# Optimization experiments

Hardware: AMD Instinct MI355X
Metric: run time of the kernel (lower is better)

Reference implementation:

```python
import jax, jax.numpy as jnp
import numpy as np

N = 100000      # nodes
F_IN = 256      # num_node_features
E = 1600000     # edges (before self-loops)
DIMS = [F_IN, 128, 100, 32, 2]  # GCNConv layer widths


def _glorot(key, fan_in, fan_out):
    s = jnp.sqrt(6.0 / (fan_in + fan_out))
    return jax.random.uniform(key, (fan_in, fan_out), jnp.float32, -s, s)


def setup_inputs() -> dict:
    key = jax.random.key(0)
    ks = jax.random.split(key, 10)
    x = jax.random.normal(ks[0], (N, F_IN), jnp.float32)
    edge_index = jax.random.randint(ks[1], (2, E), 0, N, jnp.int32)
    inp = {"x": x, "edge_index": edge_index}
    for i in range(4):
        inp[f"W{i+1}"] = _glorot(ks[2 + 2 * i], DIMS[i], DIMS[i + 1])
        inp[f"b{i+1}"] = jnp.zeros((DIMS[i + 1],), jnp.float32)
    return inp


def reference(x, edge_index, W1, b1, W2, b2, W3, b3, W4, b4):
    n = x.shape[0]
    loops = jnp.arange(n, dtype=edge_index.dtype)
    src = jnp.concatenate([edge_index[0], loops])  # [E+N]
    dst = jnp.concatenate([edge_index[1], loops])
    # symmetric normalization: deg^-1/2[src] * deg^-1/2[dst] (self-loops included)
    deg = jax.ops.segment_sum(jnp.ones_like(src, x.dtype), dst, num_segments=n)
    dis = jax.lax.rsqrt(jnp.maximum(deg, 1.0))
    norm = (dis[src] * dis[dst])[:, None]  # [E+N, 1]

    def conv(h, W, b):
        h = h @ W                                      # [N, out]
        msg = h[src] * norm                            # gather + scale [E+N, out]
        return jax.ops.segment_sum(msg, dst, num_segments=n) + b

    h = jax.nn.leaky_relu(conv(x, W1, b1), negative_slope=0.1)
    h = jax.nn.leaky_relu(conv(h, W2, b2), negative_slope=0.1)
    h = jax.nn.leaky_relu(conv(h, W3, b3), negative_slope=0.1)
    h = conv(h, W4, b4)
    return jax.nn.softmax(h, axis=-1)
```

## Files before the change

### kernel.cpp

```cpp
#include <hip/hip_runtime.h>
#include <math.h>


typedef unsigned short ushort_t;
typedef unsigned int   uint_t;
typedef short  bf16x8 __attribute__((ext_vector_type(8)));
typedef float  f32x4  __attribute__((ext_vector_type(4)));

#define BKT_SHIFT 8
#define BKT_CAP   5120
#define BIN_CHUNK 4096

__device__ __forceinline__ ushort_t f2bf(float f) {
    union { float f; uint_t u; } v; v.f = f;
    uint_t u = v.u;
    u += 0x7fffu + ((u >> 16) & 1u);
    return (ushort_t)(u >> 16);
}
__device__ __forceinline__ float bflo(uint_t u) {
    union { uint_t q; float f; } v; v.q = u << 16; return v.f;
}
__device__ __forceinline__ float bfhi(uint_t u) {
    union { uint_t q; float f; } v; v.q = u & 0xffff0000u; return v.f;
}


__global__ __launch_bounds__(256) void bin_kernel(const int* __restrict__ srcArr,
                                                  const int* __restrict__ dstArr,
                                                  int* __restrict__ bkt_cursor,
                                                  uint2* __restrict__ staging,
                                                  int E, int nb) {
    __shared__ int hist[512];
    __shared__ int base[512];
    for (int b = threadIdx.x; b < 512; b += 256) hist[b] = 0;
    __syncthreads();
    const int e0 = blockIdx.x * BIN_CHUNK;
    #pragma unroll 4
    for (int k = 0; k < BIN_CHUNK / 256; ++k) {
        int e = e0 + k * 256 + threadIdx.x;
        if (e < E) atomicAdd(&hist[dstArr[e] >> BKT_SHIFT], 1);
    }
    __syncthreads();
    for (int b = threadIdx.x; b < nb; b += 256) {
        int h = hist[b];
        base[b] = h ? atomicAdd(&bkt_cursor[b], h) : 0;
    }
    __syncthreads();
    for (int b = threadIdx.x; b < 512; b += 256) hist[b] = 0;
    __syncthreads();
    #pragma unroll 4
    for (int k = 0; k < BIN_CHUNK / 256; ++k) {
        int e = e0 + k * 256 + threadIdx.x;
        if (e < E) {
            int s = srcArr[e], d = dstArr[e];
            int b = d >> BKT_SHIFT;
            int p = atomicAdd(&hist[b], 1);
            int idx = base[b] + p;
            if (idx < BKT_CAP)
                staging[(size_t)b * BKT_CAP + idx] = make_uint2((uint_t)s, (uint_t)d);
        }
    }
}

__global__ __launch_bounds__(512) void bucket_scan_kernel(const int* __restrict__ bkt_cursor,
                                                          int* __restrict__ bkt_base,
                                                          int* __restrict__ row_start,
                                                          int nbkt, int n) {
    __shared__ int buf[512];
    int v = ((int)threadIdx.x < nbkt) ? min(bkt_cursor[threadIdx.x], BKT_CAP) : 0;
    buf[threadIdx.x] = v;
    __syncthreads();
    for (int off = 1; off < 512; off <<= 1) {
        int t = (threadIdx.x >= (unsigned)off) ? buf[threadIdx.x - off] : 0;
        __syncthreads();
        buf[threadIdx.x] += t;
        __syncthreads();
    }
    if ((int)threadIdx.x < nbkt) bkt_base[threadIdx.x] = buf[threadIdx.x] - v;
    if ((int)threadIdx.x == nbkt - 1) row_start[n] = buf[threadIdx.x];
}

__global__ __launch_bounds__(256) void csr_build2_kernel(const uint2* __restrict__ staging,
                                                         const int* __restrict__ bkt_cursor,
                                                         const int* __restrict__ bkt_base,
                                                         int* __restrict__ row_start,
                                                         float* __restrict__ dis,
                                                         int* __restrict__ csr_src, int n) {
    __shared__ int cnt[256];
    __shared__ int buf[256];
    __shared__ int rsS[256];
    __shared__ int seg[BKT_CAP];
    const int t  = threadIdx.x;
    const int b  = blockIdx.x;
    const int lo = b << BKT_SHIFT;
    const int nl = min(256, n - lo);
    cnt[t] = 0;
    __syncthreads();
    const int cntE = min(bkt_cursor[b], BKT_CAP);
    for (int e = t; e < cntE; e += 256) {
        uint2 p = staging[(size_t)b * BKT_CAP + e];
        atomicAdd(&cnt[(int)p.y - lo], 1);
    }
    __syncthreads();
    const int v = cnt[t];
    buf[t] = v;
    __syncthreads();
    for (int off = 1; off < 256; off <<= 1) {
        int tt = (t >= off) ? buf[t - off] : 0;
        __syncthreads();
        buf[t] += tt;
        __syncthreads();
    }
    rsS[t] = buf[t] - v;
    const int sbase = bkt_base[b];
    if (t < nl) {
        row_start[lo + t] = sbase + (buf[t] - v);
        dis[lo + t] = rsqrtf((float)(v + 1));
    }
    cnt[t] = 0;
    __syncthreads();
    for (int e = t; e < cntE; e += 256) {
        uint2 p = staging[(size_t)b * BKT_CAP + e];
        int ln = (int)p.y - lo;
        int q  = atomicAdd(&cnt[ln], 1);
        seg[rsS[ln] + q] = (int)p.x;
    }
    __syncthreads();
    for (int i = t; i < cntE; i += 256) csr_src[sbase + i] = seg[i];
}


__global__ void cast_bf16_kernel(const float* __restrict__ in, ushort_t* __restrict__ out, int n8) {
    int i = blockIdx.x * blockDim.x + threadIdx.x;
    if (i >= n8) return;
    const float4 f0 = ((const float4*)in)[2 * i];
    const float4 f1 = ((const float4*)in)[2 * i + 1];
    uint4 o;
    o.x = (uint_t)f2bf(f0.x) | ((uint_t)f2bf(f0.y) << 16);
    o.y = (uint_t)f2bf(f0.z) | ((uint_t)f2bf(f0.w) << 16);
    o.z = (uint_t)f2bf(f1.x) | ((uint_t)f2bf(f1.y) << 16);
    o.w = (uint_t)f2bf(f1.z) | ((uint_t)f2bf(f1.w) << 16);
    ((uint4*)out)[i] = o;
}

__global__ void wt_all_kernel(const float* __restrict__ W1, const float* __restrict__ W2,
                              const float* __restrict__ W3,
                              ushort_t* __restrict__ Wt1, ushort_t* __restrict__ Wt2,
                              ushort_t* __restrict__ Wt3) {
    int idx = blockIdx.x * blockDim.x + threadIdx.x;
    if (idx < 32768) {
        int nn = idx >> 8, k = idx & 255;
        Wt1[idx] = f2bf(W1[(size_t)k * 128 + nn]);
    } else if (idx < 49152) {
        int j = idx - 32768;
        int nn = j >> 7, k = j & 127;
        float v = (nn < 100) ? W2[(size_t)k * 100 + nn] : 0.f;
        Wt2[j] = f2bf(v);
    } else if (idx < 57344) {
        int j = idx - 49152;
        int nn = j >> 7, k = j & 127;
        float v = (k < 100 && nn < 32) ? W3[(size_t)k * 32 + nn] : 0.f;
        Wt3[j] = f2bf(v);
    }
}

template <int NFR>
__global__ __launch_bounds__(256) void gemm_tile(const ushort_t* __restrict__ A,
                                                 const ushort_t* __restrict__ Bt,
                                                 ushort_t* __restrict__ C,
                                                 const float* __restrict__ dis,
                                                 int M, int K, int lda, int ldb, int ldc) {
    constexpr int BN = NFR * 32;
    __shared__ __attribute__((aligned(16))) ushort_t As[64][72];
    __shared__ __attribute__((aligned(16))) ushort_t Bs[BN][72];

    const int t    = threadIdx.x;
    const int lane = t & 63;
    const int w    = t >> 6;
    const int wm   = w >> 1, wn = w & 1;
    const int m0   = blockIdx.x * 64;
    const int rsel = lane & 15;
    const int q    = lane >> 4;

    f32x4 acc[2][NFR];
    #pragma unroll
    for (int mi = 0; mi < 2; ++mi)
        #pragma unroll
        for (int ni = 0; ni < NFR; ++ni) acc[mi][ni] = (f32x4){0.f, 0.f, 0.f, 0.f};

    const int srow = t >> 3;
    const int scol = (t & 7) * 8;

    for (int k0 = 0; k0 < K; k0 += 64) {
        #pragma unroll
        for (int it = 0; it < 2; ++it) {
            int r = srow + it * 32;
            int gm = m0 + r;
            bf16x8 v = {0, 0, 0, 0, 0, 0, 0, 0};
            if (gm < M) v = *(const bf16x8*)(A + (size_t)gm * lda + k0 + scol);
            *(bf16x8*)&As[r][scol] = v;
        }
        #pragma unroll
        for (int it = 0; it < BN / 32; ++it) {
            int r = srow + it * 32;
            bf16x8 v = *(const bf16x8*)(Bt + (size_t)r * ldb + k0 + scol);
            *(bf16x8*)&Bs[r][scol] = v;
        }
        __syncthreads();
        #pragma unroll
        for (int ks = 0; ks < 2; ++ks) {
            const int kc = ks * 32 + q * 8;
            bf16x8 af[2], bfr[NFR];
            #pragma unroll
            for (int mi = 0; mi < 2; ++mi)
                af[mi] = *(const bf16x8*)&As[wm * 32 + mi * 16 + rsel][kc];
            #pragma unroll
            for (int ni = 0; ni < NFR; ++ni)
                bfr[ni] = *(const bf16x8*)&Bs[wn * (BN / 2) + ni * 16 + rsel][kc];
            #pragma unroll
            for (int mi = 0; mi < 2; ++mi)
                #pragma unroll
                for (int ni = 0; ni < NFR; ++ni)
                    acc[mi][ni] = __builtin_amdgcn_mfma_f32_16x16x32_bf16(
                        bfr[ni], af[mi], acc[mi][ni], 0, 0, 0);
        }
        __syncthreads();
    }

    #pragma unroll
    for (int mi = 0; mi < 2; ++mi) {
        const int gm = m0 + wm * 32 + mi * 16 + rsel;
        if (gm >= M) continue;
        const float d = dis[gm];
        #pragma unroll
        for (int ni = 0; ni < NFR; ++ni) {
            uint2 o;
            o.x = (uint_t)f2bf(acc[mi][ni][0] * d) | ((uint_t)f2bf(acc[mi][ni][1] * d) << 16);
            o.y = (uint_t)f2bf(acc[mi][ni][2] * d) | ((uint_t)f2bf(acc[mi][ni][3] * d) << 16);
            *(uint2*)(C + (size_t)gm * ldc + wn * (BN / 2) + ni * 16 + q * 4) = o;
        }
    }
}

template <int F>
__global__ void aggregate128_kernel(const ushort_t* __restrict__ h, const int* __restrict__ row_start,
                                    const int* __restrict__ csr_src,
                                    const float* __restrict__ dis, const float* __restrict__ bias,
                                    ushort_t* __restrict__ out, int n) {
    const int lane = threadIdx.x & 63;
    const int grp  = lane >> 4;
    const int node = blockIdx.x * 16 + (int)(threadIdx.x >> 6) * 4 + grp;
    if (node >= n) return;
    const uint_t fbb = (uint_t)(lane & 15) << 4;
    const char* hb = (const char*)h;
    float a[8];
    #pragma unroll
    for (int j = 0; j < 8; ++j) a[j] = 0.f;

    int i = row_start[node];
    const int end = row_start[node + 1];

#define LOADR(S) (*(const uint4*)(hb + (((uint_t)(S) << 8) + fbb)))
#define ACC8(U)                                                     \
    do {                                                            \
        a[0] += bflo((U).x); a[1] += bfhi((U).x);                   \
        a[2] += bflo((U).y); a[3] += bfhi((U).y);                   \
        a[4] += bflo((U).z); a[5] += bfhi((U).z);                   \
        a[6] += bflo((U).w); a[7] += bfhi((U).w);                   \
    } while (0)

    for (; i + 4 <= end; i += 4) {
        int s0 = csr_src[i];
        int s1 = csr_src[i + 1];
        int s2 = csr_src[i + 2];
        int s3 = csr_src[i + 3];
        uint4 u0 = LOADR(s0);
        uint4 u1 = LOADR(s1);
        uint4 u2 = LOADR(s2);
        uint4 u3 = LOADR(s3);
        ACC8(u0); ACC8(u1); ACC8(u2); ACC8(u3);
    }
    for (; i < end; ++i) {
        uint4 u = LOADR(csr_src[i]);
        ACC8(u);
    }
    {
        uint4 su = LOADR(node);
        ACC8(su);
    }
    float dn = dis[node];
    const int fb = (lane & 15) * 8;
    #pragma unroll
    for (int j = 0; j < 8; ++j) {
        float b = (fb + j < F) ? bias[fb + j] : 0.f;
        float v = a[j] * dn + b;
        v = (v > 0.f) ? v : 0.1f * v;
        if (fb + j >= F) v = 0.f;
        a[j] = v;
    }
    uint4 o;
    o.x = (uint_t)f2bf(a[0]) | ((uint_t)f2bf(a[1]) << 16);
    o.y = (uint_t)f2bf(a[2]) | ((uint_t)f2bf(a[3]) << 16);
    o.z = (uint_t)f2bf(a[4]) | ((uint_t)f2bf(a[5]) << 16);
    o.w = (uint_t)f2bf(a[6]) | ((uint_t)f2bf(a[7]) << 16);
    *(uint4*)((char*)out + (((uint_t)node << 8) + fbb)) = o;
#undef ACC8
#undef LOADR
}

__global__ void aggregate32_kernel(const ushort_t* __restrict__ h, const int* __restrict__ row_start,
                                   const int* __restrict__ csr_src,
                                   const float* __restrict__ dis, const float* __restrict__ bias,
                                   ushort_t* __restrict__ out, int n) {
    int lane16 = threadIdx.x & 15;
    int node = blockIdx.x * (blockDim.x >> 4) + (threadIdx.x >> 4);
    if (node >= n) return;
    const uint_t fbb = (uint_t)lane16 << 2;
    const char* hb = (const char*)h;
#define LOADR32(S) (*(const uint_t*)(hb + (((uint_t)(S) << 6) + fbb)))
    uint_t v = LOADR32(node);
    float acc0 = bflo(v);
    float acc1 = bfhi(v);
    int i = row_start[node], end = row_start[node + 1];
    for (; i + 4 <= end; i += 4) {
        uint_t u0 = LOADR32(csr_src[i]);
        uint_t u1 = LOADR32(csr_src[i + 1]);
        uint_t u2 = LOADR32(csr_src[i + 2]);
        uint_t u3 = LOADR32(csr_src[i + 3]);
        acc0 += bflo(u0) + bflo(u1) + bflo(u2) + bflo(u3);
        acc1 += bfhi(u0) + bfhi(u1) + bfhi(u2) + bfhi(u3);
    }
    for (; i < end; ++i) {
        uint_t u = LOADR32(csr_src[i]);
        acc0 += bflo(u); acc1 += bfhi(u);
    }
#undef LOADR32
    float dn = dis[node];
    const int f0 = 2 * lane16;
    acc0 = acc0 * dn + bias[f0];
    acc1 = acc1 * dn + bias[f0 + 1];
    acc0 = (acc0 > 0.f) ? acc0 : 0.1f * acc0;
    acc1 = (acc1 > 0.f) ? acc1 : 0.1f * acc1;
    uint_t o = (uint_t)f2bf(acc0) | ((uint_t)f2bf(acc1) << 16);
    *(uint_t*)((char*)out + (((uint_t)node << 6) + fbb)) = o;
}

__global__ void gemm32x2_kernel(const ushort_t* __restrict__ H, const float* __restrict__ W4,
                                const float* __restrict__ dis, float* __restrict__ C, int n) {
    int node = blockIdx.x * blockDim.x + threadIdx.x;
    if (node >= n) return;
    const uint_t* row = (const uint_t*)(H + (size_t)node * 32);
    float a0 = 0.f, a1 = 0.f;
    #pragma unroll
    for (int k2 = 0; k2 < 16; ++k2) {
        uint_t u = row[k2];
        float x0 = bflo(u), x1 = bfhi(u);
        int k = 2 * k2;
        a0 += x0 * W4[k * 2]     + x1 * W4[(k + 1) * 2];
        a1 += x0 * W4[k * 2 + 1] + x1 * W4[(k + 1) * 2 + 1];
    }
    float d = dis[node];
    C[2 * (size_t)node]     = a0 * d;
    C[2 * (size_t)node + 1] = a1 * d;
}

__global__ void aggregate2_softmax_kernel(const float* __restrict__ h, const int* __restrict__ row_start,
                                          const int* __restrict__ csr_src,
                                          const float* __restrict__ dis, const float* __restrict__ bias,
                                          float* __restrict__ out, int n) {
    int node = blockIdx.x * blockDim.x + threadIdx.x;
    if (node >= n) return;
    const char* hb = (const char*)h;
    float a0 = h[2 * (size_t)node];
    float a1 = h[2 * (size_t)node + 1];
    int beg = row_start[node], end = row_start[node + 1];
    for (int i = beg; i < end; ++i) {
        uint_t off = (uint_t)csr_src[i] << 3;
        float2 u = *(const float2*)(hb + off);
        a0 += u.x;
        a1 += u.y;
    }
    float dn = dis[node];
    a0 = a0 * dn + bias[0];
    a1 = a1 * dn + bias[1];
    float m  = fmaxf(a0, a1);
    float e0 = expf(a0 - m), e1 = expf(a1 - m);
    float inv = 1.f / (e0 + e1);
    out[2 * (size_t)node]     = e0 * inv;
    out[2 * (size_t)node + 1] = e1 * inv;
}


extern "C" void kernel_launch(void* const* d_in, const int* in_sizes, int n_in,
                              void* d_out, int out_size, void* d_ws, size_t ws_size,
                              hipStream_t stream) {
    const float* x  = (const float*)d_in[0];
    const int*   ei = (const int*)d_in[1];
    const float* W1 = (const float*)d_in[2];
    const float* b1 = (const float*)d_in[3];
    const float* W2 = (const float*)d_in[4];
    const float* b2 = (const float*)d_in[5];
    const float* W3 = (const float*)d_in[6];
    const float* b3 = (const float*)d_in[7];
    const float* W4 = (const float*)d_in[8];
    const float* b4 = (const float*)d_in[9];

    const int N = in_sizes[0] / 256;
    const int E = in_sizes[1] / 2;
    const int* srcA = ei;
    const int* dstA = ei + E;
    const int nbkt = (N + 255) >> BKT_SHIFT;

    char* ws = (char*)d_ws;
    size_t off = 0;
    auto alloc = [&](size_t bytes) {
        void* p = ws + off;
        off = (off + bytes + 255) & ~(size_t)255;
        return p;
    };
    float*    dis        = (float*)alloc((size_t)N * 4);
    int*      row_start  = (int*)alloc((size_t)(N + 1) * 4);
    int*      bkt_cursor = (int*)alloc(512 * 4);
    int*      bkt_base   = (int*)alloc(512 * 4);
    int*      csr_src    = (int*)alloc((size_t)E * 4);
    uint2*    staging    = (uint2*)alloc((size_t)nbkt * BKT_CAP * 8);
    ushort_t* xb         = (ushort_t*)alloc((size_t)N * 256 * 2);
    ushort_t* bufA       = (ushort_t*)alloc((size_t)N * 128 * 2);
    ushort_t* bufB       = (ushort_t*)alloc((size_t)N * 128 * 2);
    float*    C4         = (float*)alloc((size_t)N * 2 * 4);
    ushort_t* Wt1        = (ushort_t*)alloc((size_t)128 * 256 * 2);
    ushort_t* Wt2        = (ushort_t*)alloc((size_t)128 * 128 * 2);
    ushort_t* Wt3        = (ushort_t*)alloc((size_t)64 * 128 * 2);
    (void)ws_size;

    hipMemsetAsync(bkt_cursor, 0, 512 * 4, stream);

    bin_kernel<<<(E + BIN_CHUNK - 1) / BIN_CHUNK, 256, 0, stream>>>(
        srcA, dstA, bkt_cursor, staging, E, nbkt);
    bucket_scan_kernel<<<1, 512, 0, stream>>>(bkt_cursor, bkt_base, row_start, nbkt, N);
    csr_build2_kernel<<<nbkt, 256, 0, stream>>>(staging, bkt_cursor, bkt_base,
                                                row_start, dis, csr_src, N);

    wt_all_kernel<<<(57344 + 255) / 256, 256, 0, stream>>>(W1, W2, W3, Wt1, Wt2, Wt3);
    const int n8 = N * 32;
    cast_bf16_kernel<<<(n8 + 255) / 256, 256, 0, stream>>>(x, xb, n8);

    const int gx = (N + 63) / 64;
    const int aggBlocks128 = (N + 15) / 16;
    const int aggBlocks32  = (N + 15) / 16;

    gemm_tile<4><<<gx, 256, 0, stream>>>(xb, Wt1, bufA, dis, N, 256, 256, 256, 128);
    aggregate128_kernel<128><<<aggBlocks128, 256, 0, stream>>>(
        bufA, row_start, csr_src, dis, b1, bufB, N);
    gemm_tile<4><<<gx, 256, 0, stream>>>(bufB, Wt2, bufA, dis, N, 128, 128, 128, 128);
    aggregate128_kernel<100><<<aggBlocks128, 256, 0, stream>>>(
        bufA, row_start, csr_src, dis, b2, bufB, N);
    gemm_tile<1><<<gx, 256, 0, stream>>>(bufB, Wt3, bufA, dis, N, 128, 128, 128, 32);
    aggregate32_kernel<<<aggBlocks32, 256, 0, stream>>>(
        bufA, row_start, csr_src, dis, b3, bufB, N);
    gemm32x2_kernel<<<(N + 255) / 256, 256, 0, stream>>>(bufB, W4, dis, C4, N);
    aggregate2_softmax_kernel<<<(N + 255) / 256, 256, 0, stream>>>(
        C4, row_start, csr_src, dis, b4, (float*)d_out, N);
}
```

Baseline: 299.3 us.

## Fuse fp32-to-bf16 cast into first GEMM, pack staging edges, unroll gathers

```diff
diff --git a/kernel.cpp b/kernel.cpp
--- a/kernel.cpp
+++ b/kernel.cpp
@@ -28,17 +28,24 @@
 __global__ __launch_bounds__(256) void bin_kernel(const int* __restrict__ srcArr,
                                                   const int* __restrict__ dstArr,
                                                   int* __restrict__ bkt_cursor,
-                                                  uint2* __restrict__ staging,
+                                                  uint_t* __restrict__ staging,
                                                   int E, int nb) {
     __shared__ int hist[512];
     __shared__ int base[512];
     for (int b = threadIdx.x; b < 512; b += 256) hist[b] = 0;
     __syncthreads();
     const int e0 = blockIdx.x * BIN_CHUNK;
-    #pragma unroll 4
-    for (int k = 0; k < BIN_CHUNK / 256; ++k) {
+    int sv[16], dv[16];
+    #pragma unroll
+    for (int k = 0; k < 16; ++k) {
         int e = e0 + k * 256 + threadIdx.x;
-        if (e < E) atomicAdd(&hist[dstArr[e] >> BKT_SHIFT], 1);
+        if (e < E) {
+            sv[k] = srcArr[e];
+            dv[k] = dstArr[e];
+            atomicAdd(&hist[dv[k] >> BKT_SHIFT], 1);
+        } else {
+            sv[k] = 0; dv[k] = -1;
+        }
     }
     __syncthreads();
     for (int b = threadIdx.x; b < nb; b += 256) {
@@ -48,16 +55,15 @@
     __syncthreads();
     for (int b = threadIdx.x; b < 512; b += 256) hist[b] = 0;
     __syncthreads();
-    #pragma unroll 4
-    for (int k = 0; k < BIN_CHUNK / 256; ++k) {
-        int e = e0 + k * 256 + threadIdx.x;
-        if (e < E) {
-            int s = srcArr[e], d = dstArr[e];
-            int b = d >> BKT_SHIFT;
+    #pragma unroll
+    for (int k = 0; k < 16; ++k) {
+        if (dv[k] >= 0) {
+            int b = dv[k] >> BKT_SHIFT;
             int p = atomicAdd(&hist[b], 1);
             int idx = base[b] + p;
             if (idx < BKT_CAP)
-                staging[(size_t)b * BKT_CAP + idx] = make_uint2((uint_t)s, (uint_t)d);
+                staging[(size_t)b * BKT_CAP + idx] =
+                    ((uint_t)sv[k] << 8) | (uint_t)(dv[k] & 255);
         }
     }
 }
@@ -80,7 +86,7 @@
     if ((int)threadIdx.x == nbkt - 1) row_start[n] = buf[threadIdx.x];
 }
 
-__global__ __launch_bounds__(256) void csr_build2_kernel(const uint2* __restrict__ staging,
+__global__ __launch_bounds__(256) void csr_build2_kernel(const uint_t* __restrict__ staging,
                                                          const int* __restrict__ bkt_cursor,
                                                          const int* __restrict__ bkt_base,
                                                          int* __restrict__ row_start,
@@ -98,8 +104,8 @@
     __syncthreads();
     const int cntE = min(bkt_cursor[b], BKT_CAP);
     for (int e = t; e < cntE; e += 256) {
-        uint2 p = staging[(size_t)b * BKT_CAP + e];
-        atomicAdd(&cnt[(int)p.y - lo], 1);
+        uint_t p = staging[(size_t)b * BKT_CAP + e];
+        atomicAdd(&cnt[p & 255u], 1);
     }
     __syncthreads();
     const int v = cnt[t];
@@ -120,27 +126,13 @@
     cnt[t] = 0;
     __syncthreads();
     for (int e = t; e < cntE; e += 256) {
-        uint2 p = staging[(size_t)b * BKT_CAP + e];
-        int ln = (int)p.y - lo;
+        uint_t p = staging[(size_t)b * BKT_CAP + e];
+        int ln = (int)(p & 255u);
         int q  = atomicAdd(&cnt[ln], 1);
-        seg[rsS[ln] + q] = (int)p.x;
+        seg[rsS[ln] + q] = (int)(p >> 8);
     }
     __syncthreads();
     for (int i = t; i < cntE; i += 256) csr_src[sbase + i] = seg[i];
-}
-
-
-__global__ void cast_bf16_kernel(const float* __restrict__ in, ushort_t* __restrict__ out, int n8) {
-    int i = blockIdx.x * blockDim.x + threadIdx.x;
-    if (i >= n8) return;
-    const float4 f0 = ((const float4*)in)[2 * i];
-    const float4 f1 = ((const float4*)in)[2 * i + 1];
-    uint4 o;
-    o.x = (uint_t)f2bf(f0.x) | ((uint_t)f2bf(f0.y) << 16);
-    o.y = (uint_t)f2bf(f0.z) | ((uint_t)f2bf(f0.w) << 16);
-    o.z = (uint_t)f2bf(f1.x) | ((uint_t)f2bf(f1.y) << 16);
-    o.w = (uint_t)f2bf(f1.z) | ((uint_t)f2bf(f1.w) << 16);
-    ((uint4*)out)[i] = o;
 }
 
 __global__ void wt_all_kernel(const float* __restrict__ W1, const float* __restrict__ W2,
@@ -164,8 +156,8 @@
     }
 }
 
-template <int NFR>
-__global__ __launch_bounds__(256) void gemm_tile(const ushort_t* __restrict__ A,
+template <bool A_FP32, int NFR>
+__global__ __launch_bounds__(256) void gemm_tile(const void* __restrict__ Av,
                                                  const ushort_t* __restrict__ Bt,
                                                  ushort_t* __restrict__ C,
                                                  const float* __restrict__ dis,
@@ -197,7 +189,19 @@
             int r = srow + it * 32;
             int gm = m0 + r;
             bf16x8 v = {0, 0, 0, 0, 0, 0, 0, 0};
-            if (gm < M) v = *(const bf16x8*)(A + (size_t)gm * lda + k0 + scol);
+            if (gm < M) {
+                if (A_FP32) {
+                    const float* A = (const float*)Av;
+                    const float4 f0 = *(const float4*)(A + (size_t)gm * lda + k0 + scol);
+                    const float4 f1 = *(const float4*)(A + (size_t)gm * lda + k0 + scol + 4);
+                    ushort_t o[8] = { f2bf(f0.x), f2bf(f0.y), f2bf(f0.z), f2bf(f0.w),
+                                      f2bf(f1.x), f2bf(f1.y), f2bf(f1.z), f2bf(f1.w) };
+                    v = *(const bf16x8*)o;
+                } else {
+                    const ushort_t* A = (const ushort_t*)Av;
+                    v = *(const bf16x8*)(A + (size_t)gm * lda + k0 + scol);
+                }
+            }
             *(bf16x8*)&As[r][scol] = v;
         }
         #pragma unroll
@@ -269,6 +273,26 @@
         a[6] += bflo((U).w); a[7] += bfhi((U).w);                   \
     } while (0)
 
+    for (; i + 8 <= end; i += 8) {
+        int s0 = csr_src[i];
+        int s1 = csr_src[i + 1];
+        int s2 = csr_src[i + 2];
+        int s3 = csr_src[i + 3];
+        int s4 = csr_src[i + 4];
+        int s5 = csr_src[i + 5];
+        int s6 = csr_src[i + 6];
+        int s7 = csr_src[i + 7];
+        uint4 u0 = LOADR(s0);
+        uint4 u1 = LOADR(s1);
+        uint4 u2 = LOADR(s2);
+        uint4 u3 = LOADR(s3);
+        uint4 u4 = LOADR(s4);
+        uint4 u5 = LOADR(s5);
+        uint4 u6 = LOADR(s6);
+        uint4 u7 = LOADR(s7);
+        ACC8(u0); ACC8(u1); ACC8(u2); ACC8(u3);
+        ACC8(u4); ACC8(u5); ACC8(u6); ACC8(u7);
+    }
     for (; i + 4 <= end; i += 4) {
         int s0 = csr_src[i];
         int s1 = csr_src[i + 1];
@@ -423,8 +447,7 @@
     int*      bkt_cursor = (int*)alloc(512 * 4);
     int*      bkt_base   = (int*)alloc(512 * 4);
     int*      csr_src    = (int*)alloc((size_t)E * 4);
-    uint2*    staging    = (uint2*)alloc((size_t)nbkt * BKT_CAP * 8);
-    ushort_t* xb         = (ushort_t*)alloc((size_t)N * 256 * 2);
+    uint_t*   staging    = (uint_t*)alloc((size_t)nbkt * BKT_CAP * 4);
     ushort_t* bufA       = (ushort_t*)alloc((size_t)N * 128 * 2);
     ushort_t* bufB       = (ushort_t*)alloc((size_t)N * 128 * 2);
     float*    C4         = (float*)alloc((size_t)N * 2 * 4);
@@ -442,20 +465,18 @@
                                                 row_start, dis, csr_src, N);
 
     wt_all_kernel<<<(57344 + 255) / 256, 256, 0, stream>>>(W1, W2, W3, Wt1, Wt2, Wt3);
-    const int n8 = N * 32;
-    cast_bf16_kernel<<<(n8 + 255) / 256, 256, 0, stream>>>(x, xb, n8);
 
     const int gx = (N + 63) / 64;
     const int aggBlocks128 = (N + 15) / 16;
     const int aggBlocks32  = (N + 15) / 16;
 
-    gemm_tile<4><<<gx, 256, 0, stream>>>(xb, Wt1, bufA, dis, N, 256, 256, 256, 128);
+    gemm_tile<true, 4><<<gx, 256, 0, stream>>>(x, Wt1, bufA, dis, N, 256, 256, 256, 128);
     aggregate128_kernel<128><<<aggBlocks128, 256, 0, stream>>>(
         bufA, row_start, csr_src, dis, b1, bufB, N);
-    gemm_tile<4><<<gx, 256, 0, stream>>>(bufB, Wt2, bufA, dis, N, 128, 128, 128, 128);
+    gemm_tile<false, 4><<<gx, 256, 0, stream>>>(bufB, Wt2, bufA, dis, N, 128, 128, 128, 128);
     aggregate128_kernel<100><<<aggBlocks128, 256, 0, stream>>>(
         bufA, row_start, csr_src, dis, b2, bufB, N);
-    gemm_tile<1><<<gx, 256, 0, stream>>>(bufB, Wt3, bufA, dis, N, 128, 128, 128, 32);
+    gemm_tile<false, 1><<<gx, 256, 0, stream>>>(bufB, Wt3, bufA, dis, N, 128, 128, 128, 32);
     aggregate32_kernel<<<aggBlocks32, 256, 0, stream>>>(
         bufA, row_start, csr_src, dis, b3, bufB, N);
     gemm32x2_kernel<<<(N + 255) / 256, 256, 0, stream>>>(bufB, W4, dis, C4, N);
```

After: 279.2 us, median of 2. -6.7%, faster.
